# Kernel optimization log

Measured on AMD Instinct MI355X. Metric: run time of the kernel, lower is better.

The kernel has to match this reference:

```python
import jax, jax.numpy as jnp
import numpy as np

B, W, C, C2, K_DIV = 4, 64, 256, 256, 8
DPROJ = C // K_DIV  # 32


def setup_inputs() -> dict:
    key = jax.random.key(0)
    k1, k2, k3, k4 = jax.random.split(key, 4)
    x = jax.random.normal(k1, (B, W, W, C), dtype=jnp.float32)
    input_h = jax.random.normal(k2, (B, W, W, C2), dtype=jnp.float32)
    f_w = jax.random.normal(k3, (1, 1, C2, DPROJ), dtype=jnp.float32) * 0.05
    g_w = jax.random.normal(k4, (1, 1, C, DPROJ), dtype=jnp.float32) * 0.05
    return {"x": x, "input_h": input_h, "f_w": f_w, "g_w": g_w}


def reference(x, input_h, f_w, g_w):
    b, w, _, c = x.shape
    c2 = input_h.shape[-1]
    # 1x1 convs == channel matmuls
    f = jnp.einsum('bhwc,cd->bhwd', input_h, f_w[0, 0])   # [B,W,W,Dp]
    g = jnp.einsum('bhwc,cd->bhwd', x, g_w[0, 0])          # [B,W,W,Dp]
    gf = g.reshape(b, w * w, -1)                            # [B,N,Dp]
    ff = f.reshape(b, w * w, -1)                            # [B,N,Dp]
    s = jnp.einsum('bnd,bmd->bnm', gf, ff)                  # unscaled QK^T
    beta = jax.nn.softmax(s, axis=-1)
    hf = input_h.reshape(b, w * w, c2)                      # [B,N,C2]
    o = jnp.einsum('bnm,bmc->bnc', beta, hf).reshape(b, w, w, c2)
    return jnp.concatenate([o, x], axis=-1)                 # [B,W,W,C2+C]
```

## Files before the change

### kernel.cpp

```cpp
#include <hip/hip_runtime.h>
#include <hip/hip_bf16.h>

#define NB   4
#define NROW 4096
#define CIN  256
#define OUTC 512
#define DP   32

typedef __bf16 bf16x8 __attribute__((ext_vector_type(8)));
typedef float  f32x4  __attribute__((ext_vector_type(4)));
typedef ushort ushort8 __attribute__((ext_vector_type(8)));

__device__ __forceinline__ ushort f2bf(float x) {
  union { float f; unsigned u; } v; v.f = x;
  unsigned r = v.u + 0x7fffu + ((v.u >> 16) & 1u);
  return (ushort)(r >> 16);
}

__device__ __forceinline__ uint pack2(float a, float b) {
  __hip_bfloat162 h = __float22bfloat162_rn(float2{a, b});
  uint u; __builtin_memcpy(&u, &h, 4);
  return u;
}

__device__ __forceinline__ void gload_lds16(const void* g, void* l) {
  __builtin_amdgcn_global_load_lds(
      (const __attribute__((address_space(1))) unsigned int*)g,
      (__attribute__((address_space(3))) unsigned int*)l, 16, 0, 0);
}


__global__ __launch_bounds__(256) void proj_mfma(
    const float* __restrict__ x, const float* __restrict__ h,
    const float* __restrict__ fw, const float* __restrict__ gw,
    ushort* __restrict__ Qb, ushort* __restrict__ Kb, ushort* __restrict__ Vw) {
  __shared__ ushort Ab[64 * 256];
  __shared__ ushort Wt[32 * 256];
  const int t = threadIdx.x;
  const int which = blockIdx.y;
  const float* in   = which ? h : x;
  const float* wsrc = which ? fw : gw;
  ushort* dst = which ? Kb : Qb;
  const int row0 = blockIdx.x * 64;

  {
    const float4* inp = (const float4*)(in + (size_t)row0 * CIN);
#pragma unroll
    for (int i = 0; i < 16; ++i) {
      const int idx = i * 256 + t;
      const int r = idx >> 6;
      const int c = (idx & 63) * 4;
      const float4 v = inp[idx];
      ushort tmp[4] = {f2bf(v.x), f2bf(v.y), f2bf(v.z), f2bf(v.w)};
      const int slot = (c >> 3) ^ (r & 7);
      *(uint2*)&Ab[r * 256 + (slot << 3) + (c & 7)] = *(const uint2*)tmp;
    }
  }
  {
    const int d = t & 31;
    const int k0 = (t >> 5) * 32;
#pragma unroll 8
    for (int j = 0; j < 32; ++j)
      Wt[d * 256 + k0 + j] = f2bf(wsrc[(size_t)(k0 + j) * DP + d]);
  }
  __syncthreads();

  const int w = t >> 6, l = t & 63, lo = l & 15, hi = l >> 4;
  f32x4 acc[2];
  acc[0] = (f32x4){0.f, 0.f, 0.f, 0.f};
  acc[1] = (f32x4){0.f, 0.f, 0.f, 0.f};
  const int R = w * 16 + lo;
#pragma unroll
  for (int kk = 0; kk < 8; ++kk) {
    const int slot = (kk * 4 + hi) ^ (R & 7);
    const bf16x8 a = *(const bf16x8*)&Ab[R * 256 + (slot << 3)];
#pragma unroll
    for (int nt = 0; nt < 2; ++nt) {
      const bf16x8 bfr = *(const bf16x8*)&Wt[(nt * 16 + lo) * 256 + kk * 32 + hi * 8];
      acc[nt] = __builtin_amdgcn_mfma_f32_16x16x32_bf16(a, bfr, acc[nt], 0, 0, 0);
    }
  }
#pragma unroll
  for (int nt = 0; nt < 2; ++nt)
#pragma unroll
    for (int r = 0; r < 4; ++r)
      dst[(size_t)(row0 + w * 16 + hi * 4 + r) * DP + nt * 16 + lo] = f2bf(acc[nt][r]);

  if (which) {
    const int b = row0 >> 12;
    const int tile = (row0 & 4095) >> 6;
    const int c = t;
    ushort* vdst = Vw + ((size_t)(b * 64 + tile) * 256 + c) * 64;
#pragma unroll
    for (int g = 0; g < 8; ++g) {
      ushort tmp[8];
#pragma unroll
      for (int j = 0; j < 8; ++j) {
        const int slot = (c >> 3) ^ j;
        tmp[j] = Ab[(8 * g + j) * 256 + (slot << 3) + (c & 7)];
      }
      *(ushort8*)(vdst + ((g ^ (c & 7)) << 3)) = *(const ushort8*)tmp;
    }
  }
}

__global__ __launch_bounds__(512, 4) void attn8(
    const ushort* __restrict__ Qb, const ushort* __restrict__ Kb,
    const ushort* __restrict__ Vw, float* __restrict__ pml,
    ushort* __restrict__ pacc) {
  __shared__ ushort Vt[2][16384];
  __shared__ uint   Pl[4096];

  const int t  = threadIdx.x;
  const int w  = t >> 6;
  const int l  = t & 63;
  const int lo = l & 15;
  const int hi = l >> 4;

  const int bid = blockIdx.x;
  const int s   = bid & 3;
  const int b   = (bid >> 2) & 3;
  const int qsb = bid >> 4;
  const int qrow = qsb * 128 + w * 16;
  const size_t rbase = (size_t)b * NROW;

  const bf16x8 qf = *(const bf16x8*)(Qb + (rbase + qrow + lo) * DP + hi * 8);

  f32x4 acc[16];
#pragma unroll
  for (int i = 0; i < 16; ++i) acc[i] = (f32x4){0.f, 0.f, 0.f, 0.f};
  float mrow = -1e30f, lsum = 0.f;

  uint* plw = Pl + w * 512;
  const int tI0 = s * 16;

  {
    const ushort* src = Vw + (size_t)(b * 64 + tI0) * 16384;
#pragma unroll
    for (int i = 0; i < 4; ++i)
      gload_lds16(src + (w * 4 + i) * 512 + l * 8, &Vt[0][(w * 4 + i) * 512]);
  }
  bf16x8 kf[4];
#pragma unroll
  for (int kt = 0; kt < 4; ++kt)
    kf[kt] = *(const bf16x8*)(Kb + (rbase + tI0 * 64 + kt * 16 + lo) * DP + hi * 8);
  __syncthreads();
  int cur = 0;

  for (int tt = 0; tt < 16; ++tt) {
    const int tileIdx = tI0 + tt;

    if (tt < 15) {
      const ushort* src = Vw + (size_t)(b * 64 + tileIdx + 1) * 16384;
#pragma unroll
      for (int i = 0; i < 4; ++i)
        gload_lds16(src + (w * 4 + i) * 512 + l * 8, &Vt[cur ^ 1][(w * 4 + i) * 512]);
    }

    f32x4 st[4];
#pragma unroll
    for (int kt = 0; kt < 4; ++kt)
      st[kt] = __builtin_amdgcn_mfma_f32_16x16x32_bf16(
          kf[kt], qf, (f32x4){0.f, 0.f, 0.f, 0.f}, 0, 0, 0);

    float m4 = -1e30f;
#pragma unroll
    for (int kt = 0; kt < 4; ++kt)
#pragma unroll
      for (int r = 0; r < 4; ++r) m4 = fmaxf(m4, st[kt][r]);
    m4 = fmaxf(m4, __shfl_xor(m4, 16, 64));
    m4 = fmaxf(m4, __shfl_xor(m4, 32, 64));
    if (__any(m4 > mrow + 5.f)) {
      const float mn = fmaxf(mrow, m4);
      const float alpha = __expf(mrow - mn);
      mrow = mn;
#pragma unroll
      for (int ct = 0; ct < 16; ++ct) acc[ct] *= alpha;
      lsum *= alpha;
    }
    float ps = 0.f;
#pragma unroll
    for (int kt = 0; kt < 4; ++kt)
#pragma unroll
      for (int r = 0; r < 4; ++r) {
        const float p = __expf(st[kt][r] - mrow);
        st[kt][r] = p;
        ps += p;
      }
    ps += __shfl_xor(ps, 16, 64);
    ps += __shfl_xor(ps, 32, 64);
    lsum += ps;

#pragma unroll
    for (int kt = 0; kt < 4; ++kt)
#pragma unroll
      for (int pr = 0; pr < 2; ++pr) {
        const uint pd = pack2(st[kt][2 * pr], st[kt][2 * pr + 1]);
        plw[lo * 32 + ((((kt << 1) + (hi >> 1)) ^ (lo & 7)) << 2) +
            ((hi & 1) << 1) + pr] = pd;
      }

    const int tN = (tt < 15) ? tileIdx + 1 : tileIdx;
#pragma unroll
    for (int kt = 0; kt < 4; ++kt)
      kf[kt] = *(const bf16x8*)(Kb + (rbase + tN * 64 + kt * 16 + lo) * DP + hi * 8);

    const bf16x8 pb0 = *(const bf16x8*)&plw[lo * 32 + ((hi ^ (lo & 7)) << 2)];
    const bf16x8 pb1 = *(const bf16x8*)&plw[lo * 32 + (((hi + 4) ^ (lo & 7)) << 2)];
    const ushort* vb = Vt[cur];
    __builtin_amdgcn_s_setprio(1);
#pragma unroll
    for (int ct = 0; ct < 16; ++ct) {
      const int c = ct * 16 + lo;
      const bf16x8 v0 = *(const bf16x8*)&vb[c * 64 + ((hi ^ (c & 7)) << 3)];
      const bf16x8 v1 = *(const bf16x8*)&vb[c * 64 + (((hi + 4) ^ (c & 7)) << 3)];
      acc[ct] = __builtin_amdgcn_mfma_f32_16x16x32_bf16(v0, pb0, acc[ct], 0, 0, 0);
      acc[ct] = __builtin_amdgcn_mfma_f32_16x16x32_bf16(v1, pb1, acc[ct], 0, 0, 0);
    }
    __builtin_amdgcn_s_setprio(0);

    __syncthreads();
    cur ^= 1;
  }

  const size_t prow = rbase + qrow + lo;
  if (hi == 0) {
    float* mlp = pml + (prow * 4 + s) * 2;
    mlp[0] = mrow;
    mlp[1] = lsum;
  }
  ushort* pr = pacc + (prow * 4 + s) * 256;
#pragma unroll
  for (int ct = 0; ct < 16; ++ct) {
    uint2 d;
    d.x = pack2(acc[ct][0], acc[ct][1]);
    d.y = pack2(acc[ct][2], acc[ct][3]);
    *(uint2*)&pr[ct * 16 + (hi << 2)] = d;
  }
}

__global__ __launch_bounds__(256) void reduce_concat(
    const float* __restrict__ pml, const ushort* __restrict__ pacc,
    const float* __restrict__ x, float* __restrict__ out) {
  const int t = threadIdx.x;
  const int row = blockIdx.x * 8 + (t >> 5);
  const int c0 = (t & 31) * 8;

  float ms[4], ls[4];
  float m = -1e30f;
#pragma unroll
  for (int s = 0; s < 4; ++s) {
    ms[s] = pml[((size_t)row * 4 + s) * 2];
    ls[s] = pml[((size_t)row * 4 + s) * 2 + 1];
    m = fmaxf(m, ms[s]);
  }
  float L = 0.f, wgt[4];
#pragma unroll
  for (int s = 0; s < 4; ++s) {
    wgt[s] = __expf(ms[s] - m);
    L += wgt[s] * ls[s];
  }
  float o[8] = {0.f, 0.f, 0.f, 0.f, 0.f, 0.f, 0.f, 0.f};
#pragma unroll
  for (int s = 0; s < 4; ++s) {
    const bf16x8 a = *(const bf16x8*)(pacc + ((size_t)row * 4 + s) * 256 + c0);
    const float wg = wgt[s];
#pragma unroll
    for (int i = 0; i < 8; ++i) o[i] += wg * (float)a[i];
  }
  const float inv = 1.f / L;
  float4 o0 = {o[0] * inv, o[1] * inv, o[2] * inv, o[3] * inv};
  float4 o1 = {o[4] * inv, o[5] * inv, o[6] * inv, o[7] * inv};
  float4* op = (float4*)(out + (size_t)row * OUTC + c0);
  op[0] = o0; op[1] = o1;
  const float4* xp = (const float4*)(x + (size_t)row * CIN + c0);
  float4* oc = (float4*)(out + (size_t)row * OUTC + 256 + c0);
  oc[0] = xp[0]; oc[1] = xp[1];
}

__global__ __launch_bounds__(256) void proj_fb(
    const float* __restrict__ x, const float* __restrict__ h,
    const float* __restrict__ fw, const float* __restrict__ gw,
    float* __restrict__ out) {
  __shared__ float wl[8192];
  __shared__ float rows[8][260];
  const int t = threadIdx.x;
  const int which = blockIdx.y;
  const float* in = which ? h : x;
  const float* w  = which ? fw : gw;
  for (int i = t; i < 8192; i += 256) wl[i] = w[i];
  const int row0 = blockIdx.x * 32;
  const int d = t & 31, rl = t >> 5;
  for (int rp = 0; rp < 4; ++rp) {
    __syncthreads();
    for (int i = t; i < 2048; i += 256)
      rows[i >> 8][i & 255] = in[(long)(row0 + rp * 8 + (i >> 8)) * CIN + (i & 255)];
    __syncthreads();
    float a = 0.f;
#pragma unroll 8
    for (int c = 0; c < 256; ++c) a = fmaf(rows[rl][c], wl[c * 32 + d], a);
    const long row = row0 + rp * 8 + rl;
    ((ushort*)(out + row * OUTC + 256))[which * 32 + d] = f2bf(a);
  }
}

__global__ __launch_bounds__(256) void attn_fb(
    const float* __restrict__ h, float* __restrict__ out) {
  __shared__ alignas(16) ushort Vt[256][72];
  __shared__ alignas(16) ushort Pl[4][16][72];
  const int t = threadIdx.x;
  const int w = t >> 6, l = t & 63, lo = l & 15, hi = l >> 4;
  const int bid = blockIdx.x;
  const int b = (bid >> 1) & 3;
  const int qb = ((bid >> 3) << 1) | (bid & 1);
  const int q0 = qb * 64;
  const long rowbase = (long)b * NROW;
  const ushort* gslot = (const ushort*)(out + (rowbase + q0 + w * 16 + lo) * OUTC + 256);
  const bf16x8 qf = *(const bf16x8*)(gslot + hi * 8);
  f32x4 acc[16];
#pragma unroll
  for (int i = 0; i < 16; ++i) acc[i] = (f32x4){0.f, 0.f, 0.f, 0.f};
  float mrow[4] = {-1e30f, -1e30f, -1e30f, -1e30f};
  float lsum[4] = {0.f, 0.f, 0.f, 0.f};
  for (int k0 = 0; k0 < NROW; k0 += 64) {
    bf16x8 kf[4];
#pragma unroll
    for (int kt = 0; kt < 4; ++kt) {
      const ushort* fslot =
          (const ushort*)(out + (rowbase + k0 + kt * 16 + lo) * OUTC + 256) + 32;
      kf[kt] = *(const bf16x8*)(fslot + hi * 8);
    }
    __syncthreads();
    {
      const float* hp = h + (rowbase + k0) * CIN + t;
#pragma unroll
      for (int g8 = 0; g8 < 8; ++g8) {
        ushort tmp[8];
#pragma unroll
        for (int i = 0; i < 8; ++i) tmp[i] = f2bf(hp[(g8 * 8 + i) * CIN]);
        *(bf16x8*)&Vt[t][g8 * 8] = *(const bf16x8*)tmp;
      }
    }
    __syncthreads();
    f32x4 sv[4];
#pragma unroll
    for (int kt = 0; kt < 4; ++kt)
      sv[kt] = __builtin_amdgcn_mfma_f32_16x16x32_bf16(
          qf, kf[kt], (f32x4){0.f, 0.f, 0.f, 0.f}, 0, 0, 0);
    float alpha[4];
    bool upd = false;
#pragma unroll
    for (int r = 0; r < 4; ++r) {
      float m4 = fmaxf(fmaxf(sv[0][r], sv[1][r]), fmaxf(sv[2][r], sv[3][r]));
#pragma unroll
      for (int off = 1; off < 16; off <<= 1) m4 = fmaxf(m4, __shfl_xor(m4, off, 64));
      const float mn = fmaxf(mrow[r], m4);
      alpha[r] = __expf(mrow[r] - mn);
      upd |= (mn > mrow[r]);
      mrow[r] = mn;
    }
    if (__any(upd)) {
#pragma unroll
      for (int ct = 0; ct < 16; ++ct)
#pragma unroll
        for (int r = 0; r < 4; ++r) acc[ct][r] *= alpha[r];
#pragma unroll
      for (int r = 0; r < 4; ++r) lsum[r] *= alpha[r];
    }
#pragma unroll
    for (int r = 0; r < 4; ++r) {
      float ps = 0.f;
#pragma unroll
      for (int kt = 0; kt < 4; ++kt) {
        const float p = __expf(sv[kt][r] - mrow[r]);
        sv[kt][r] = p;
        ps += p;
      }
#pragma unroll
      for (int off = 1; off < 16; off <<= 1) ps += __shfl_xor(ps, off, 64);
      lsum[r] += ps;
    }
#pragma unroll
    for (int kt = 0; kt < 4; ++kt)
#pragma unroll
      for (int r = 0; r < 4; ++r)
        Pl[w][hi * 4 + r][kt * 16 + lo] = f2bf(sv[kt][r]);
    asm volatile("s_waitcnt lgkmcnt(0)" ::: "memory");
    const bf16x8 pa0 = *(const bf16x8*)&Pl[w][lo][hi * 8];
    const bf16x8 pa1 = *(const bf16x8*)&Pl[w][lo][32 + hi * 8];
#pragma unroll
    for (int ct = 0; ct < 16; ++ct) {
      const bf16x8 v0 = *(const bf16x8*)&Vt[ct * 16 + lo][hi * 8];
      const bf16x8 v1 = *(const bf16x8*)&Vt[ct * 16 + lo][32 + hi * 8];
      acc[ct] = __builtin_amdgcn_mfma_f32_16x16x32_bf16(pa0, v0, acc[ct], 0, 0, 0);
      acc[ct] = __builtin_amdgcn_mfma_f32_16x16x32_bf16(pa1, v1, acc[ct], 0, 0, 0);
    }
  }
#pragma unroll
  for (int r = 0; r < 4; ++r) {
    const float inv = 1.f / lsum[r];
    float* orow = out + (rowbase + q0 + w * 16 + hi * 4 + r) * OUTC;
#pragma unroll
    for (int ct = 0; ct < 16; ++ct) orow[ct * 16 + lo] = acc[ct][r] * inv;
  }
}

__global__ __launch_bounds__(256) void concat_fb(
    const float4* __restrict__ x, float4* __restrict__ out) {
  const int idx = blockIdx.x * 256 + threadIdx.x;
  const int row = idx >> 6, c4 = idx & 63;
  out[row * 128 + 64 + c4] = x[idx];
}

extern "C" void kernel_launch(void* const* d_in, const int* in_sizes, int n_in,
                              void* d_out, int out_size, void* d_ws, size_t ws_size,
                              hipStream_t stream) {
  const float* x  = (const float*)d_in[0];
  const float* h  = (const float*)d_in[1];
  const float* fw = (const float*)d_in[2];
  const float* gw = (const float*)d_in[3];
  float* out = (float*)d_out;

  const size_t rows = (size_t)NB * NROW;
  const size_t base = 10ull * 1024 * 1024;
  const size_t need = base + rows * 4 * 8 + rows * 4 * 512;

  if (ws_size >= need) {
    ushort* Qw = (ushort*)d_ws;
    ushort* Kw = Qw + (1ull << 19);
    ushort* Vw = Kw + (1ull << 19);
    float*  pml  = (float*)((char*)d_ws + base);
    ushort* pacc = (ushort*)((char*)d_ws + base + rows * 4 * 8);

    proj_mfma<<<dim3(256, 2), 256, 0, stream>>>(x, h, fw, gw, Qw, Kw, Vw);
    attn8<<<512, 512, 0, stream>>>(Qw, Kw, Vw, pml, pacc);
    reduce_concat<<<2048, 256, 0, stream>>>(pml, pacc, x, out);
  } else {
    proj_fb<<<dim3(512, 2), 256, 0, stream>>>(x, h, fw, gw, out);
    attn_fb<<<256, 256, 0, stream>>>(h, out);
    concat_fb<<<4096, 256, 0, stream>>>((const float4*)x, (float4*)out);
  }
}
```

Measured before the change: 86.46 us.

## Switch attention to 32x32 MFMA tiles with log2e-prescaled exp2 softmax

Rewrites the attention kernel to use 32x32x16 bf16 MFMA with 4 waves of 256 threads, each wave handling 32 query rows instead of 16. Q is prescaled by log2(e) in the projection so softmax can use exp2f, with the reduce kernel matching. V staging drops from a double buffer to a single LDS buffer loaded after a barrier, which frees LDS but exposes load latency. Larger tiles cut MFMA and LDS fragment-read count per FLOP and shuffle reductions, and the rescale threshold is raised to match the new base.

```diff
diff --git a/kernel.cpp b/kernel.cpp
--- a/kernel.cpp
+++ b/kernel.cpp
@@ -6,10 +6,14 @@
 #define CIN  256
 #define OUTC 512
 #define DP   32
+#define LOG2E 1.4426950408889634f
 
 typedef __bf16 bf16x8 __attribute__((ext_vector_type(8)));
 typedef float  f32x4  __attribute__((ext_vector_type(4)));
+typedef float  f32x16 __attribute__((ext_vector_type(16)));
 typedef ushort ushort8 __attribute__((ext_vector_type(8)));
+
+#define MFMA32(a, b, c) __builtin_amdgcn_mfma_f32_32x32x16_bf16((a), (b), (c), 0, 0, 0)
 
 __device__ __forceinline__ ushort f2bf(float x) {
   union { float f; unsigned u; } v; v.f = x;
@@ -41,6 +45,7 @@
   const float* in   = which ? h : x;
   const float* wsrc = which ? fw : gw;
   ushort* dst = which ? Kb : Qb;
+  const float qsc = which ? 1.f : LOG2E;
   const int row0 = blockIdx.x * 64;
 
   {
@@ -84,7 +89,8 @@
   for (int nt = 0; nt < 2; ++nt)
 #pragma unroll
     for (int r = 0; r < 4; ++r)
-      dst[(size_t)(row0 + w * 16 + hi * 4 + r) * DP + nt * 16 + lo] = f2bf(acc[nt][r]);
+      dst[(size_t)(row0 + w * 16 + hi * 4 + r) * DP + nt * 16 + lo] =
+          f2bf(acc[nt][r] * qsc);
 
   if (which) {
     const int b = row0 >> 12;
@@ -104,139 +110,153 @@
   }
 }
 
-__global__ __launch_bounds__(512, 4) void attn8(
+__global__ __launch_bounds__(256) void attn32(
     const ushort* __restrict__ Qb, const ushort* __restrict__ Kb,
     const ushort* __restrict__ Vw, float* __restrict__ pml,
     ushort* __restrict__ pacc) {
-  __shared__ ushort Vt[2][16384];
-  __shared__ uint   Pl[4096];
+  __shared__ ushort Vt[16384];
+  __shared__ uint   Pl[4][1024];
 
   const int t  = threadIdx.x;
   const int w  = t >> 6;
   const int l  = t & 63;
-  const int lo = l & 15;
-  const int hi = l >> 4;
+  const int qq = l & 31;
+  const int h  = l >> 5;
 
   const int bid = blockIdx.x;
   const int s   = bid & 3;
   const int b   = (bid >> 2) & 3;
   const int qsb = bid >> 4;
-  const int qrow = qsb * 128 + w * 16;
+  const int q0  = qsb * 128 + w * 32;
   const size_t rbase = (size_t)b * NROW;
 
-  const bf16x8 qf = *(const bf16x8*)(Qb + (rbase + qrow + lo) * DP + hi * 8);
-
-  f32x4 acc[16];
-#pragma unroll
-  for (int i = 0; i < 16; ++i) acc[i] = (f32x4){0.f, 0.f, 0.f, 0.f};
+  bf16x8 qf[2];
+#pragma unroll
+  for (int ks = 0; ks < 2; ++ks)
+    qf[ks] = *(const bf16x8*)(Qb + (rbase + q0 + qq) * DP + ks * 16 + h * 8);
+
+  f32x16 acc[8];
+#pragma unroll
+  for (int i = 0; i < 8; ++i) acc[i] = (f32x16){};
   float mrow = -1e30f, lsum = 0.f;
 
-  uint* plw = Pl + w * 512;
+  uint* Pp = Pl[w];
   const int tI0 = s * 16;
 
   {
     const ushort* src = Vw + (size_t)(b * 64 + tI0) * 16384;
 #pragma unroll
-    for (int i = 0; i < 4; ++i)
-      gload_lds16(src + (w * 4 + i) * 512 + l * 8, &Vt[0][(w * 4 + i) * 512]);
-  }
-  bf16x8 kf[4];
-#pragma unroll
-  for (int kt = 0; kt < 4; ++kt)
-    kf[kt] = *(const bf16x8*)(Kb + (rbase + tI0 * 64 + kt * 16 + lo) * DP + hi * 8);
-  __syncthreads();
-  int cur = 0;
+    for (int i = 0; i < 8; ++i)
+      gload_lds16(src + (w * 8 + i) * 512 + l * 8, &Vt[(w * 8 + i) * 512]);
+  }
+  bf16x8 kf[2][2];
+#pragma unroll
+  for (int e = 0; e < 2; ++e)
+#pragma unroll
+    for (int ks = 0; ks < 2; ++ks)
+      kf[e][ks] = *(const bf16x8*)(Kb + (rbase + tI0 * 64 + e * 32 + qq) * DP +
+                                   ks * 16 + h * 8);
 
   for (int tt = 0; tt < 16; ++tt) {
-    const int tileIdx = tI0 + tt;
-
-    if (tt < 15) {
-      const ushort* src = Vw + (size_t)(b * 64 + tileIdx + 1) * 16384;
-#pragma unroll
-      for (int i = 0; i < 4; ++i)
-        gload_lds16(src + (w * 4 + i) * 512 + l * 8, &Vt[cur ^ 1][(w * 4 + i) * 512]);
-    }
-
-    f32x4 st[4];
-#pragma unroll
-    for (int kt = 0; kt < 4; ++kt)
-      st[kt] = __builtin_amdgcn_mfma_f32_16x16x32_bf16(
-          kf[kt], qf, (f32x4){0.f, 0.f, 0.f, 0.f}, 0, 0, 0);
-
-    float m4 = -1e30f;
-#pragma unroll
-    for (int kt = 0; kt < 4; ++kt)
-#pragma unroll
-      for (int r = 0; r < 4; ++r) m4 = fmaxf(m4, st[kt][r]);
-    m4 = fmaxf(m4, __shfl_xor(m4, 16, 64));
+    f32x16 st0 = (f32x16){}, st1 = (f32x16){};
+    st0 = MFMA32(kf[0][0], qf[0], st0);
+    st0 = MFMA32(kf[0][1], qf[1], st0);
+    st1 = MFMA32(kf[1][0], qf[0], st1);
+    st1 = MFMA32(kf[1][1], qf[1], st1);
+
+    float m4 = st0[0];
+#pragma unroll
+    for (int i = 1; i < 16; ++i) m4 = fmaxf(m4, st0[i]);
+#pragma unroll
+    for (int i = 0; i < 16; ++i) m4 = fmaxf(m4, st1[i]);
     m4 = fmaxf(m4, __shfl_xor(m4, 32, 64));
-    if (__any(m4 > mrow + 5.f)) {
+    if (__any(m4 > mrow + 7.f)) {
       const float mn = fmaxf(mrow, m4);
-      const float alpha = __expf(mrow - mn);
+      const float alpha = exp2f(mrow - mn);
       mrow = mn;
 #pragma unroll
-      for (int ct = 0; ct < 16; ++ct) acc[ct] *= alpha;
+      for (int ct = 0; ct < 8; ++ct) acc[ct] *= alpha;
       lsum *= alpha;
     }
     float ps = 0.f;
 #pragma unroll
-    for (int kt = 0; kt < 4; ++kt)
-#pragma unroll
-      for (int r = 0; r < 4; ++r) {
-        const float p = __expf(st[kt][r] - mrow);
-        st[kt][r] = p;
-        ps += p;
-      }
-    ps += __shfl_xor(ps, 16, 64);
+    for (int i = 0; i < 16; ++i) {
+      const float p = exp2f(st0[i] - mrow); st0[i] = p; ps += p;
+    }
+#pragma unroll
+    for (int i = 0; i < 16; ++i) {
+      const float p = exp2f(st1[i] - mrow); st1[i] = p; ps += p;
+    }
     ps += __shfl_xor(ps, 32, 64);
     lsum += ps;
 
 #pragma unroll
+    for (int j = 0; j < 4; ++j) {
+      uint2 d0, d1;
+      d0.x = pack2(st0[4 * j], st0[4 * j + 1]);
+      d0.y = pack2(st0[4 * j + 2], st0[4 * j + 3]);
+      d1.x = pack2(st1[4 * j], st1[4 * j + 1]);
+      d1.y = pack2(st1[4 * j + 2], st1[4 * j + 3]);
+      *(uint2*)&Pp[qq * 32 + ((j ^ (qq & 7)) << 2) + h * 2] = d0;
+      *(uint2*)&Pp[qq * 32 + (((4 + j) ^ (qq & 7)) << 2) + h * 2] = d1;
+    }
+
+    if (tt < 15) {
+      const size_t kb = rbase + (size_t)(tI0 + tt + 1) * 64;
+#pragma unroll
+      for (int e = 0; e < 2; ++e)
+#pragma unroll
+        for (int ks = 0; ks < 2; ++ks)
+          kf[e][ks] = *(const bf16x8*)(Kb + (kb + e * 32 + qq) * DP + ks * 16 + h * 8);
+    }
+
+    __syncthreads();
+
+    bf16x8 pb[4];
+#pragma unroll
     for (int kt = 0; kt < 4; ++kt)
-#pragma unroll
-      for (int pr = 0; pr < 2; ++pr) {
-        const uint pd = pack2(st[kt][2 * pr], st[kt][2 * pr + 1]);
-        plw[lo * 32 + ((((kt << 1) + (hi >> 1)) ^ (lo & 7)) << 2) +
-            ((hi & 1) << 1) + pr] = pd;
+      pb[kt] = *(const bf16x8*)&((const ushort*)Pp)[qq * 64 +
+               ((((kt << 1) + h) ^ (qq & 7)) << 3)];
+
+    __builtin_amdgcn_s_setprio(1);
+#pragma unroll
+    for (int ct = 0; ct < 8; ++ct) {
+      const int c = ct * 32 + qq;
+#pragma unroll
+      for (int kt = 0; kt < 4; ++kt) {
+        const bf16x8 v = *(const bf16x8*)&Vt[c * 64 +
+                         ((((kt << 1) + h) ^ (c & 7)) << 3)];
+        acc[ct] = MFMA32(v, pb[kt], acc[ct]);
       }
-
-    const int tN = (tt < 15) ? tileIdx + 1 : tileIdx;
-#pragma unroll
-    for (int kt = 0; kt < 4; ++kt)
-      kf[kt] = *(const bf16x8*)(Kb + (rbase + tN * 64 + kt * 16 + lo) * DP + hi * 8);
-
-    const bf16x8 pb0 = *(const bf16x8*)&plw[lo * 32 + ((hi ^ (lo & 7)) << 2)];
-    const bf16x8 pb1 = *(const bf16x8*)&plw[lo * 32 + (((hi + 4) ^ (lo & 7)) << 2)];
-    const ushort* vb = Vt[cur];
-    __builtin_amdgcn_s_setprio(1);
-#pragma unroll
-    for (int ct = 0; ct < 16; ++ct) {
-      const int c = ct * 16 + lo;
-      const bf16x8 v0 = *(const bf16x8*)&vb[c * 64 + ((hi ^ (c & 7)) << 3)];
-      const bf16x8 v1 = *(const bf16x8*)&vb[c * 64 + (((hi + 4) ^ (c & 7)) << 3)];
-      acc[ct] = __builtin_amdgcn_mfma_f32_16x16x32_bf16(v0, pb0, acc[ct], 0, 0, 0);
-      acc[ct] = __builtin_amdgcn_mfma_f32_16x16x32_bf16(v1, pb1, acc[ct], 0, 0, 0);
     }
     __builtin_amdgcn_s_setprio(0);
 
     __syncthreads();
-    cur ^= 1;
-  }
-
-  const size_t prow = rbase + qrow + lo;
-  if (hi == 0) {
+
+    if (tt < 15) {
+      const ushort* src = Vw + (size_t)(b * 64 + tI0 + tt + 1) * 16384;
+#pragma unroll
+      for (int i = 0; i < 8; ++i)
+        gload_lds16(src + (w * 8 + i) * 512 + l * 8, &Vt[(w * 8 + i) * 512]);
+    }
+  }
+
+  const size_t prow = rbase + q0 + qq;
+  if (h == 0) {
     float* mlp = pml + (prow * 4 + s) * 2;
     mlp[0] = mrow;
     mlp[1] = lsum;
   }
   ushort* pr = pacc + (prow * 4 + s) * 256;
 #pragma unroll
-  for (int ct = 0; ct < 16; ++ct) {
-    uint2 d;
-    d.x = pack2(acc[ct][0], acc[ct][1]);
-    d.y = pack2(acc[ct][2], acc[ct][3]);
-    *(uint2*)&pr[ct * 16 + (hi << 2)] = d;
-  }
+  for (int ct = 0; ct < 8; ++ct)
+#pragma unroll
+    for (int j = 0; j < 4; ++j) {
+      uint2 d;
+      d.x = pack2(acc[ct][4 * j], acc[ct][4 * j + 1]);
+      d.y = pack2(acc[ct][4 * j + 2], acc[ct][4 * j + 3]);
+      *(uint2*)&pr[ct * 32 + j * 8 + h * 4] = d;
+    }
 }
 
 __global__ __launch_bounds__(256) void reduce_concat(
@@ -257,7 +277,7 @@
   float L = 0.f, wgt[4];
 #pragma unroll
   for (int s = 0; s < 4; ++s) {
-    wgt[s] = __expf(ms[s] - m);
+    wgt[s] = exp2f(ms[s] - m);
     L += wgt[s] * ls[s];
   }
   float o[8] = {0.f, 0.f, 0.f, 0.f, 0.f, 0.f, 0.f, 0.f};
@@ -433,7 +453,7 @@
     ushort* pacc = (ushort*)((char*)d_ws + base + rows * 4 * 8);
 
     proj_mfma<<<dim3(256, 2), 256, 0, stream>>>(x, h, fw, gw, Qw, Kw, Vw);
-    attn8<<<512, 512, 0, stream>>>(Qw, Kw, Vw, pml, pacc);
+    attn32<<<512, 256, 0, stream>>>(Qw, Kw, Vw, pml, pacc);
     reduce_concat<<<2048, 256, 0, stream>>>(pml, pacc, x, out);
   } else {
     proj_fb<<<dim3(512, 2), 256, 0, stream>>>(x, h, fw, gw, out);
```

After: 122.6 us. +41.8%, slower.
